# Kernel optimization log

Hardware: AMD Instinct MI355X
Metric: run time of the kernel (lower is better)

## Reference

```python
import jax, jax.numpy as jnp
import numpy as np

NINP = 1024
NHID = 1024
BATCH = 16384


def setup_inputs() -> dict:
    key = jax.random.key(0)
    ks = jax.random.split(key, 12)
    std = 1.0 / np.sqrt(NHID)
    u = lambda k, shape: jax.random.uniform(k, shape, jnp.float32, -std, std)
    return {
        "x": jax.random.normal(ks[0], (BATCH, NINP), jnp.float32),
        "y": jax.random.normal(ks[1], (BATCH, NHID), jnp.float32),
        "z": jax.random.normal(ks[2], (BATCH, NHID), jnp.float32),
        "dt": jax.random.uniform(ks[3], (BATCH, 1), jnp.float32),
        "W_ih": u(ks[4], (4 * NHID, NINP)),
        "b_ih": u(ks[5], (4 * NHID,)),
        "W_hh": u(ks[6], (3 * NHID, NHID)),
        "b_hh": u(ks[7], (3 * NHID,)),
        "W_z": u(ks[8], (NHID, NHID)),
        "b_z": u(ks[9], (NHID,)),
        "W_dt": u(ks[10], (2, 1)),
        "b_dt": u(ks[11], (2,)),
    }


def reference(x, y, z, dt, W_ih, b_ih, W_hh, b_hh, W_z, b_z, W_dt, b_dt):
    # transformed_inp = inp2hid(x): [B, 4H]
    ti = x @ W_ih.T + b_ih
    # transformed_hid = hid2hid(y): [B, 3H]
    th = y @ W_hh.T + b_hh
    H = NHID
    i_dt1, i_dt2, i_z, i_y = ti[:, :H], ti[:, H:2*H], ti[:, 2*H:3*H], ti[:, 3*H:]
    h_dt1, h_dt2, h_y = th[:, :H], th[:, H:2*H], th[:, 2*H:]
    tdt = dt @ W_dt.T + b_dt  # [B, 2]
    t_dt1, t_dt2 = tdt[:, 0:1], tdt[:, 1:2]
    ms_dt_bar = jax.nn.sigmoid(t_dt1) * jax.nn.sigmoid(i_dt1 + h_dt1)
    ms_dt = jax.nn.sigmoid(t_dt2) * jax.nn.sigmoid(i_dt2 + h_dt2)
    z_new = (1.0 - ms_dt) * z + ms_dt * jnp.tanh(i_y + h_y)
    y_new = (1.0 - ms_dt_bar) * y + ms_dt_bar * jnp.tanh(z_new @ W_z.T + b_z + i_z)
    return (y_new, z_new)
```

## Files before the change

### kernel.cpp

```cpp
#include <hip/hip_runtime.h>
#include <hip/hip_bf16.h>

#define BATCH 16384
#define HDIM  1024
#define K1    2048

typedef __attribute__((ext_vector_type(4))) float f32x4;
typedef __attribute__((ext_vector_type(4))) int i32x4;
typedef __attribute__((ext_vector_type(8))) short short8;

__device__ __forceinline__ unsigned short f2bf(float f) {
  union { float f; unsigned u; } v; v.f = f;
  unsigned r = v.u + 0x7FFFu + ((v.u >> 16) & 1u);
  return (unsigned short)(r >> 16);
}
__device__ __forceinline__ float bf2f(unsigned short h) {
  union { unsigned u; float f; } v; v.u = ((unsigned)h) << 16; return v.f;
}
__device__ __forceinline__ float sigmoidf_(float x) {
  return 1.0f / (1.0f + __builtin_amdgcn_exp2f(x * -1.4426950408889634f));
}
__device__ __forceinline__ float tanhf_(float x) {
  float xc = fminf(fmaxf(x, -8.0f), 8.0f);
  float e = __builtin_amdgcn_exp2f(xc * 2.8853900817779268f);
  return (e - 1.0f) / (e + 1.0f);
}
__device__ __forceinline__ void async16(const void* g, void* l) {
  __builtin_amdgcn_global_load_lds((const __attribute__((address_space(1))) void*)g,
                                   (__attribute__((address_space(3))) void*)l, 16, 0, 0);
}
__device__ __forceinline__ int q8p(float4 v, float s) {
  int a = __float2int_rn(fminf(fmaxf(v.x * s, -127.f), 127.f));
  int b = __float2int_rn(fminf(fmaxf(v.y * s, -127.f), 127.f));
  int c = __float2int_rn(fminf(fmaxf(v.z * s, -127.f), 127.f));
  int d = __float2int_rn(fminf(fmaxf(v.w * s, -127.f), 127.f));
  return (a & 255) | ((b & 255) << 8) | ((c & 255) << 16) | ((d & 255) << 24);
}

#define QXS (127.0f / 6.0f)
#define QWS (127.0f / 0.03125f)
#define SXW ((6.0f / 127.0f) * (0.03125f / 127.0f))

__global__ void k_conv(const float* __restrict__ x, const float* __restrict__ y,
                       const float* __restrict__ Wih, const float* __restrict__ Whh,
                       const float* __restrict__ Wz,
                       char* __restrict__ U8, unsigned short* __restrict__ Xbf,
                       char* __restrict__ W8, unsigned short* __restrict__ Wzcat) {
  const int stride = gridDim.x * blockDim.x;
  const int tid0 = blockIdx.x * blockDim.x + threadIdx.x;
  const int totalU = BATCH * (HDIM / 4);
  for (int q = tid0; q < totalU; q += stride) {
    int b = q >> 8;
    int c = (q & 255) << 2;
    float4 xv = *(const float4*)(x + (long)b * HDIM + c);
    float4 yv = *(const float4*)(y + (long)b * HDIM + c);
    *(int*)(U8 + (long)b * K1 + c) = q8p(xv, QXS);
    *(int*)(U8 + (long)b * K1 + HDIM + c) = q8p(yv, QXS);
    uint2 xo;
    xo.x = (unsigned)f2bf(xv.x) | ((unsigned)f2bf(xv.y) << 16);
    xo.y = (unsigned)f2bf(xv.z) | ((unsigned)f2bf(xv.w) << 16);
    *(uint2*)(Xbf + (long)b * HDIM + c) = xo;
  }
  const int totalW = 3072 * (K1 / 4);
  for (int q = tid0; q < totalW; q += stride) {
    int np = q >> 9;
    int kb = (q & 511) << 2;
    int bn = np / 192; int r = np - bn * 192;
    int w = r / 48; int r2 = r - w * 48;
    int c = r2 >> 4, i = r2 & 15;
    int h = bn * 64 + w * 16 + i;
    float4 v;
    if (kb < HDIM) {
      int row = (c == 0) ? h : (c == 1) ? (HDIM + h) : (3 * HDIM + h);
      v = *(const float4*)(Wih + (long)row * HDIM + kb);
    } else {
      int row = (c == 0) ? h : (c == 1) ? (HDIM + h) : (2 * HDIM + h);
      v = *(const float4*)(Whh + (long)row * HDIM + (kb - HDIM));
    }
    *(int*)(W8 + (long)np * K1 + kb) = q8p(v, QWS);
  }
  const int totalZ = HDIM * (K1 / 4);
  for (int q = tid0; q < totalZ; q += stride) {
    int n = q >> 9;
    int kb = (q & 511) << 2;
    float4 v = (kb < HDIM) ? *(const float4*)(Wz + (long)n * HDIM + kb)
                           : *(const float4*)(Wih + (long)(2 * HDIM + n) * HDIM + (kb - HDIM));
    uint2 o;
    o.x = (unsigned)f2bf(v.x) | ((unsigned)f2bf(v.y) << 16);
    o.y = (unsigned)f2bf(v.z) | ((unsigned)f2bf(v.w) << 16);
    *(uint2*)(Wzcat + (long)n * K1 + kb) = o;
  }
}

__global__ __launch_bounds__(512, 2) void k_gemm1(
    const char* __restrict__ U8, const char* __restrict__ W8,
    const float* __restrict__ z, const float* __restrict__ dtp,
    const float* __restrict__ bih, const float* __restrict__ bhh,
    const float* __restrict__ Wdt, const float* __restrict__ bdt,
    float* __restrict__ out, unsigned short* __restrict__ znb,
    unsigned short* __restrict__ sbb) {
  __shared__ char lds[114688];
  char* ldsA = lds;
  char* ldsB = lds + 65536;
  const int bid = blockIdx.x;
  const int sid = (bid & 7) * 128 + (bid >> 3);
  const int bm = sid >> 4, bn = sid & 15;
  const long arow0 = (long)bm * 256, brow0 = (long)bn * 192;
  constexpr int NT = 32;

  const int t = threadIdx.x, lane = t & 63, wv = t >> 6;
  const int wm = wv >> 2, wn = wv & 3;
  const int rA = lane & 15;
  const int cphys = ((lane >> 4) << 4) ^ (((rA >> 1) & 3) << 4);
  const int t16 = t * 16;
  const bool blo = (t < 256);

  const int sA = t16 ^ (((t16 >> 7) & 3) << 4);
  const int rA0 = sA >> 6, cA0 = sA & 63;
  const char* pAa = U8 + (arow0 + rA0) * (long)K1 + cA0;
  const char* pAb = U8 + (arow0 + rA0 + 128) * (long)K1 + cA0;

  const int Lb0 = blo ? t16 : t16 + 4096;
  const int Lb1 = t16 + 4096;
  const int sB0 = Lb0 ^ (((Lb0 >> 7) & 3) << 4);
  const int sB1 = Lb1 ^ (((Lb1 >> 7) & 3) << 4);
  const char* pBg0 = W8 + (brow0 + (sB0 >> 6)) * (long)K1 + (sB0 & 63);
  const char* pBg1 = W8 + (brow0 + (sB1 >> 6)) * (long)K1 + (sB1 & 63);

  int offA[8], offB[3];
#pragma unroll
  for (int m = 0; m < 8; ++m)
    offA[m] = (wm * 128 + m * 16 + rA) * 64 + cphys;
#pragma unroll
  for (int n = 0; n < 3; ++n)
    offB[n] = (wn * 48 + n * 16 + rA) * 64 + cphys;

#define STAGE_(TT)                                                        \
  do {                                                                    \
    char* ab_ = ldsA + ((TT) & 3) * 16384;                                \
    char* bb_ = ldsB + ((TT) & 3) * 12288;                                \
    async16(pAa + (long)(TT) * 64, ab_ + t16);                            \
    async16(pAb + (long)(TT) * 64, ab_ + 8192 + t16);                     \
    async16(pBg0 + (long)(TT) * 64, bb_ + Lb0);                           \
    if (blo) async16(pBg1 + (long)(TT) * 64, bb_ + Lb1);                  \
  } while (0)
#define WSTEADY_                                                          \
  do {                                                                    \
    if (blo) asm volatile("s_waitcnt vmcnt(8) lgkmcnt(0)" ::: "memory");  \
    else     asm volatile("s_waitcnt vmcnt(6) lgkmcnt(0)" ::: "memory");  \
  } while (0)
#define WTAIL1_                                                           \
  do {                                                                    \
    if (blo) asm volatile("s_waitcnt vmcnt(4) lgkmcnt(0)" ::: "memory");  \
    else     asm volatile("s_waitcnt vmcnt(3) lgkmcnt(0)" ::: "memory");  \
  } while (0)
#define WTAIL0_ asm volatile("s_waitcnt vmcnt(0) lgkmcnt(0)" ::: "memory")
#define WLAST_  asm volatile("s_waitcnt lgkmcnt(0)" ::: "memory")

  i32x4 acc[8][3];
#pragma unroll
  for (int m = 0; m < 8; ++m)
#pragma unroll
    for (int n = 0; n < 3; ++n) acc[m][n] = (i32x4)(0);

  STAGE_(0);
  STAGE_(1);
  STAGE_(2);
  WSTEADY_;
  __builtin_amdgcn_s_barrier();

#pragma unroll 1
  for (int kt = 0; kt < NT; ++kt) {
    const char* Ab_ = ldsA + (kt & 3) * 16384;
    const char* Bb_ = ldsB + (kt & 3) * 12288;
    i32x4 af_[8], bf_[3];
#pragma unroll
    for (int m = 0; m < 8; ++m) af_[m] = *(const i32x4*)(Ab_ + offA[m]);
#pragma unroll
    for (int n = 0; n < 3; ++n) bf_[n] = *(const i32x4*)(Bb_ + offB[n]);
    if (kt < NT - 3) {
      STAGE_(kt + 3);
      WSTEADY_;
    } else if (kt == NT - 3) {
      WTAIL1_;
    } else if (kt == NT - 2) {
      WTAIL0_;
    } else {
      WLAST_;
    }
    __builtin_amdgcn_s_barrier();
    __builtin_amdgcn_sched_barrier(0);
    __builtin_amdgcn_s_setprio(1);
#pragma unroll
    for (int m = 0; m < 8; ++m)
#pragma unroll
      for (int n = 0; n < 3; ++n)
        acc[m][n] = __builtin_amdgcn_mfma_i32_16x16x64_i8(
            af_[m], bf_[n], acc[m][n], 0, 0, 0);
    __builtin_amdgcn_s_setprio(0);
  }
#undef STAGE_
#undef WSTEADY_
#undef WTAIL1_
#undef WTAIL0_
#undef WLAST_

  const int q4 = (lane >> 4) << 2;
  const int h = bn * 64 + wn * 16 + rA;
  const int rowbase = bm * 256 + wm * 128;
  const float bi0 = bih[h] + bhh[h];
  const float bi1 = bih[HDIM + h] + bhh[HDIM + h];
  const float bi2 = bih[3 * HDIM + h] + bhh[2 * HDIM + h];
  const float wdt0 = Wdt[0], wdt1 = Wdt[1], bdt0 = bdt[0], bdt1 = bdt[1];
#pragma unroll
  for (int m = 0; m < 8; ++m) {
#pragma unroll
    for (int j = 0; j < 4; ++j) {
      const int b = rowbase + m * 16 + q4 + j;
      const long idx = (long)b * HDIM + h;
      const float dv = dtp[b];
      const float s1 = sigmoidf_(dv * wdt0 + bdt0);
      const float s2 = sigmoidf_(dv * wdt1 + bdt1);
      const float g0 = (float)acc[m][0][j] * SXW + bi0;
      const float g1 = (float)acc[m][1][j] * SXW + bi1;
      const float g2 = (float)acc[m][2][j] * SXW + bi2;
      const float sbar = s1 * sigmoidf_(g0);
      const float s = s2 * sigmoidf_(g1);
      const float zt = tanhf_(g2);
      const float znew = (1.0f - s) * z[idx] + s * zt;
      out[(long)BATCH * HDIM + idx] = znew;
      znb[idx] = f2bf(znew);
      sbb[idx] = f2bf(sbar);
    }
  }
}

template <int NB, int KSPLIT>
__device__ __forceinline__ void gemm_core(
    const unsigned short* __restrict__ A1, int strA1,
    const unsigned short* __restrict__ A2, int strA2,
    const unsigned short* __restrict__ Bg,
    long arow0, long brow0, char* lds, f32x4 acc[8][NB]) {
  constexpr int NT = 64;
  constexpr int BBY = NB * 4096;
  char* ldsA = lds;
  char* ldsB = lds + 65536;
  const int t = threadIdx.x, lane = t & 63, wv = t >> 6;
  const int wm = wv >> 2, wn = wv & 3;
  const int rA = lane & 15;
  const int cphys = ((lane >> 4) << 4) ^ (((rA >> 1) & 3) << 4);
  const int t16 = t * 16;

  const int sA = t16 ^ (((t16 >> 7) & 3) << 4);
  const int rA0 = sA >> 6, cA0 = (sA & 63) >> 1;
  const unsigned short* pA1a = A1 + (arow0 + rA0) * (long)strA1 + cA0;
  const unsigned short* pA1b = A1 + (arow0 + rA0 + 128) * (long)strA1 + cA0;
  const unsigned short* pA2a = A2 + (arow0 + rA0) * (long)strA2 + cA0;
  const unsigned short* pA2b = A2 + (arow0 + rA0 + 128) * (long)strA2 + cA0;

  const int Lb0 = t16;
  const int sB0 = Lb0 ^ (((Lb0 >> 7) & 3) << 4);
  const unsigned short* pBg0 = Bg + (brow0 + (sB0 >> 6)) * (long)K1 + ((sB0 & 63) >> 1);

  int offA[8], offB[NB];
#pragma unroll
  for (int m = 0; m < 8; ++m)
    offA[m] = (wm * 128 + m * 16 + rA) * 64 + cphys;
#pragma unroll
  for (int n = 0; n < NB; ++n)
    offB[n] = (wn * (NB * 16) + n * 16 + rA) * 64 + cphys;

#define STAGE2_(TT)                                                       \
  do {                                                                    \
    char* ab_ = ldsA + ((TT) & 3) * 16384;                                \
    char* bb_ = ldsB + ((TT) & 3) * BBY;                                  \
    if ((TT) < KSPLIT) {                                                  \
      async16(pA1a + (long)(TT) * 32, ab_ + t16);                         \
      async16(pA1b + (long)(TT) * 32, ab_ + 8192 + t16);                  \
    } else {                                                              \
      async16(pA2a + (long)((TT) - KSPLIT) * 32, ab_ + t16);              \
      async16(pA2b + (long)((TT) - KSPLIT) * 32, ab_ + 8192 + t16);       \
    }                                                                     \
    async16(pBg0 + (long)(TT) * 32, bb_ + Lb0);                           \
  } while (0)
#define W2S_ asm volatile("s_waitcnt vmcnt(6) lgkmcnt(0)" ::: "memory")
#define W2A_ asm volatile("s_waitcnt vmcnt(3) lgkmcnt(0)" ::: "memory")
#define W2B_ asm volatile("s_waitcnt vmcnt(0) lgkmcnt(0)" ::: "memory")
#define W2C_ asm volatile("s_waitcnt lgkmcnt(0)" ::: "memory")

  STAGE2_(0);
  STAGE2_(1);
  STAGE2_(2);
  W2S_;
  __builtin_amdgcn_s_barrier();

#pragma unroll 1
  for (int kt = 0; kt < NT; ++kt) {
    const char* Ab_ = ldsA + (kt & 3) * 16384;
    const char* Bb_ = ldsB + (kt & 3) * BBY;
    short8 af_[8], bf_[NB];
#pragma unroll
    for (int m = 0; m < 8; ++m) af_[m] = *(const short8*)(Ab_ + offA[m]);
#pragma unroll
    for (int n = 0; n < NB; ++n) bf_[n] = *(const short8*)(Bb_ + offB[n]);
    if (kt < NT - 3) {
      STAGE2_(kt + 3);
      W2S_;
    } else if (kt == NT - 3) {
      W2A_;
    } else if (kt == NT - 2) {
      W2B_;
    } else {
      W2C_;
    }
    __builtin_amdgcn_s_barrier();
    __builtin_amdgcn_sched_barrier(0);
    __builtin_amdgcn_s_setprio(1);
#pragma unroll
    for (int m = 0; m < 8; ++m)
#pragma unroll
      for (int n = 0; n < NB; ++n)
        acc[m][n] = __builtin_amdgcn_mfma_f32_16x16x32_bf16(
            af_[m], bf_[n], acc[m][n], 0, 0, 0);
    __builtin_amdgcn_s_setprio(0);
  }
#undef STAGE2_
#undef W2S_
#undef W2A_
#undef W2B_
#undef W2C_
}

__global__ __launch_bounds__(512, 2) void k_gemm2(
    const unsigned short* __restrict__ Zn, const unsigned short* __restrict__ Xbf,
    const unsigned short* __restrict__ Wzcat, const unsigned short* __restrict__ sbb,
    const float* __restrict__ yin, const float* __restrict__ bz,
    float* __restrict__ out) {
  __shared__ char lds[98304];
  const int bid = blockIdx.x;
  const int sid = (bid & 7) * 64 + (bid >> 3);
  const int bm = sid >> 3, bn = sid & 7;
  f32x4 acc[8][2];
#pragma unroll
  for (int m = 0; m < 8; ++m)
#pragma unroll
    for (int n = 0; n < 2; ++n) acc[m][n] = (f32x4)(0.0f);

  gemm_core<2, 32>(Zn, HDIM, Xbf, HDIM, Wzcat, (long)bm * 256, (long)bn * 128, lds, acc);

  const int t = threadIdx.x, lane = t & 63, wv = t >> 6;
  const int wm = wv >> 2, wn = wv & 3;
  const int rA = lane & 15, q4 = (lane >> 4) << 2;
  const int rowbase = bm * 256 + wm * 128;
#pragma unroll
  for (int n = 0; n < 2; ++n) {
    const int hc = bn * 128 + wn * 32 + n * 16 + rA;
    const float bzv = bz[hc];
#pragma unroll
    for (int m = 0; m < 8; ++m) {
#pragma unroll
      for (int j = 0; j < 4; ++j) {
        const int b = rowbase + m * 16 + q4 + j;
        const long idx = (long)b * HDIM + hc;
        const float tv = tanhf_(acc[m][n][j] + bzv);
        const float sb = bf2f(sbb[idx]);
        out[idx] = (1.0f - sb) * yin[idx] + sb * tv;
      }
    }
  }
}

extern "C" void kernel_launch(void* const* d_in, const int* in_sizes, int n_in,
                              void* d_out, int out_size, void* d_ws, size_t ws_size,
                              hipStream_t stream) {
  const float* x   = (const float*)d_in[0];
  const float* y   = (const float*)d_in[1];
  const float* z   = (const float*)d_in[2];
  const float* dtp = (const float*)d_in[3];
  const float* Wih = (const float*)d_in[4];
  const float* bih = (const float*)d_in[5];
  const float* Whh = (const float*)d_in[6];
  const float* bhh = (const float*)d_in[7];
  const float* Wz  = (const float*)d_in[8];
  const float* bz  = (const float*)d_in[9];
  const float* Wdt = (const float*)d_in[10];
  const float* bdt = (const float*)d_in[11];

  char* ws = (char*)d_ws;
  char*           U8    = ws;
  unsigned short* Xbf   = (unsigned short*)(ws + 33554432);
  char*           W8    = ws + 67108864;
  unsigned short* Wzcat = (unsigned short*)(ws + 73400320);
  unsigned short* Znb   = (unsigned short*)(ws + 77594624);
  unsigned short* Sbb   = (unsigned short*)(ws + 111149056);
  float* out = (float*)d_out;

  k_conv<<<2048, 256, 0, stream>>>(x, y, Wih, Whh, Wz, U8, Xbf, W8, Wzcat);
  k_gemm1<<<1024, 512, 0, stream>>>(U8, W8, z, dtp, bih, bhh, Wdt, bdt, out, Znb, Sbb);
  k_gemm2<<<512, 512, 0, stream>>>(Znb, Xbf, Wzcat, Sbb, y, bz, out);
}
```

Baseline: 324.9 us.

## Switch second GEMM to int8 MFMA and reuse quantized x from first GEMM

```diff
diff --git a/kernel.cpp b/kernel.cpp
--- a/kernel.cpp
+++ b/kernel.cpp
@@ -7,7 +7,6 @@
 
 typedef __attribute__((ext_vector_type(4))) float f32x4;
 typedef __attribute__((ext_vector_type(4))) int i32x4;
-typedef __attribute__((ext_vector_type(8))) short short8;
 
 __device__ __forceinline__ unsigned short f2bf(float f) {
   union { float f; unsigned u; } v; v.f = f;
@@ -44,8 +43,8 @@
 __global__ void k_conv(const float* __restrict__ x, const float* __restrict__ y,
                        const float* __restrict__ Wih, const float* __restrict__ Whh,
                        const float* __restrict__ Wz,
-                       char* __restrict__ U8, unsigned short* __restrict__ Xbf,
-                       char* __restrict__ W8, unsigned short* __restrict__ Wzcat) {
+                       char* __restrict__ U8, char* __restrict__ W8,
+                       char* __restrict__ Wz8) {
   const int stride = gridDim.x * blockDim.x;
   const int tid0 = blockIdx.x * blockDim.x + threadIdx.x;
   const int totalU = BATCH * (HDIM / 4);
@@ -56,10 +55,6 @@
     float4 yv = *(const float4*)(y + (long)b * HDIM + c);
     *(int*)(U8 + (long)b * K1 + c) = q8p(xv, QXS);
     *(int*)(U8 + (long)b * K1 + HDIM + c) = q8p(yv, QXS);
-    uint2 xo;
-    xo.x = (unsigned)f2bf(xv.x) | ((unsigned)f2bf(xv.y) << 16);
-    xo.y = (unsigned)f2bf(xv.z) | ((unsigned)f2bf(xv.w) << 16);
-    *(uint2*)(Xbf + (long)b * HDIM + c) = xo;
   }
   const int totalW = 3072 * (K1 / 4);
   for (int q = tid0; q < totalW; q += stride) {
@@ -85,10 +80,7 @@
     int kb = (q & 511) << 2;
     float4 v = (kb < HDIM) ? *(const float4*)(Wz + (long)n * HDIM + kb)
                            : *(const float4*)(Wih + (long)(2 * HDIM + n) * HDIM + (kb - HDIM));
-    uint2 o;
-    o.x = (unsigned)f2bf(v.x) | ((unsigned)f2bf(v.y) << 16);
-    o.y = (unsigned)f2bf(v.z) | ((unsigned)f2bf(v.w) << 16);
-    *(uint2*)(Wzcat + (long)n * K1 + kb) = o;
+    *(int*)(Wz8 + (long)n * K1 + kb) = q8p(v, QWS);
   }
 }
 
@@ -97,7 +89,7 @@
     const float* __restrict__ z, const float* __restrict__ dtp,
     const float* __restrict__ bih, const float* __restrict__ bhh,
     const float* __restrict__ Wdt, const float* __restrict__ bdt,
-    float* __restrict__ out, unsigned short* __restrict__ znb,
+    float* __restrict__ out, char* __restrict__ zn8,
     unsigned short* __restrict__ sbb) {
   __shared__ char lds[114688];
   char* ldsA = lds;
@@ -229,22 +221,27 @@
       const float zt = tanhf_(g2);
       const float znew = (1.0f - s) * z[idx] + s * zt;
       out[(long)BATCH * HDIM + idx] = znew;
-      znb[idx] = f2bf(znew);
+      int qz = __float2int_rn(fminf(fmaxf(znew * QXS, -127.f), 127.f));
+      zn8[idx] = (char)qz;
       sbb[idx] = f2bf(sbar);
     }
   }
 }
 
-template <int NB, int KSPLIT>
-__device__ __forceinline__ void gemm_core(
-    const unsigned short* __restrict__ A1, int strA1,
-    const unsigned short* __restrict__ A2, int strA2,
-    const unsigned short* __restrict__ Bg,
-    long arow0, long brow0, char* lds, f32x4 acc[8][NB]) {
-  constexpr int NT = 64;
-  constexpr int BBY = NB * 4096;
+__global__ __launch_bounds__(512, 2) void k_gemm2(
+    const char* __restrict__ Zn8, const char* __restrict__ U8,
+    const char* __restrict__ Wz8, const unsigned short* __restrict__ sbb,
+    const float* __restrict__ yin, const float* __restrict__ bz,
+    float* __restrict__ out) {
+  __shared__ char lds[98304];
   char* ldsA = lds;
   char* ldsB = lds + 65536;
+  const int bid = blockIdx.x;
+  const int sid = (bid & 7) * 64 + (bid >> 3);
+  const int bm = sid >> 3, bn = sid & 7;
+  const long arow0 = (long)bm * 256, brow0 = (long)bn * 128;
+  constexpr int NT = 32, KSPLIT = 16;
+
   const int t = threadIdx.x, lane = t & 63, wv = t >> 6;
   const int wm = wv >> 2, wn = wv & 3;
   const int rA = lane & 15;
@@ -252,42 +249,47 @@
   const int t16 = t * 16;
 
   const int sA = t16 ^ (((t16 >> 7) & 3) << 4);
-  const int rA0 = sA >> 6, cA0 = (sA & 63) >> 1;
-  const unsigned short* pA1a = A1 + (arow0 + rA0) * (long)strA1 + cA0;
-  const unsigned short* pA1b = A1 + (arow0 + rA0 + 128) * (long)strA1 + cA0;
-  const unsigned short* pA2a = A2 + (arow0 + rA0) * (long)strA2 + cA0;
-  const unsigned short* pA2b = A2 + (arow0 + rA0 + 128) * (long)strA2 + cA0;
-
-  const int Lb0 = t16;
-  const int sB0 = Lb0 ^ (((Lb0 >> 7) & 3) << 4);
-  const unsigned short* pBg0 = Bg + (brow0 + (sB0 >> 6)) * (long)K1 + ((sB0 & 63) >> 1);
-
-  int offA[8], offB[NB];
+  const int rA0 = sA >> 6, cA0 = sA & 63;
+  const char* pZa = Zn8 + (arow0 + rA0) * (long)HDIM + cA0;
+  const char* pZb = Zn8 + (arow0 + rA0 + 128) * (long)HDIM + cA0;
+  const char* pXa = U8 + (arow0 + rA0) * (long)K1 + cA0;
+  const char* pXb = U8 + (arow0 + rA0 + 128) * (long)K1 + cA0;
+
+  const int sB0 = t16 ^ (((t16 >> 7) & 3) << 4);
+  const char* pBg0 = Wz8 + (brow0 + (sB0 >> 6)) * (long)K1 + (sB0 & 63);
+
+  int offA[8], offB[2];
 #pragma unroll
   for (int m = 0; m < 8; ++m)
     offA[m] = (wm * 128 + m * 16 + rA) * 64 + cphys;
 #pragma unroll
-  for (int n = 0; n < NB; ++n)
-    offB[n] = (wn * (NB * 16) + n * 16 + rA) * 64 + cphys;
+  for (int n = 0; n < 2; ++n)
+    offB[n] = (wn * 32 + n * 16 + rA) * 64 + cphys;
 
 #define STAGE2_(TT)                                                       \
   do {                                                                    \
     char* ab_ = ldsA + ((TT) & 3) * 16384;                                \
-    char* bb_ = ldsB + ((TT) & 3) * BBY;                                  \
+    char* bb_ = ldsB + ((TT) & 3) * 8192;                                 \
     if ((TT) < KSPLIT) {                                                  \
-      async16(pA1a + (long)(TT) * 32, ab_ + t16);                         \
-      async16(pA1b + (long)(TT) * 32, ab_ + 8192 + t16);                  \
+      async16(pZa + (long)(TT) * 64, ab_ + t16);                          \
+      async16(pZb + (long)(TT) * 64, ab_ + 8192 + t16);                   \
     } else {                                                              \
-      async16(pA2a + (long)((TT) - KSPLIT) * 32, ab_ + t16);              \
-      async16(pA2b + (long)((TT) - KSPLIT) * 32, ab_ + 8192 + t16);       \
+      async16(pXa + (long)((TT) - KSPLIT) * 64, ab_ + t16);               \
+      async16(pXb + (long)((TT) - KSPLIT) * 64, ab_ + 8192 + t16);        \
     }                                                                     \
-    async16(pBg0 + (long)(TT) * 32, bb_ + Lb0);                           \
+    async16(pBg0 + (long)(TT) * 64, bb_ + t16);                           \
   } while (0)
 #define W2S_ asm volatile("s_waitcnt vmcnt(6) lgkmcnt(0)" ::: "memory")
 #define W2A_ asm volatile("s_waitcnt vmcnt(3) lgkmcnt(0)" ::: "memory")
 #define W2B_ asm volatile("s_waitcnt vmcnt(0) lgkmcnt(0)" ::: "memory")
 #define W2C_ asm volatile("s_waitcnt lgkmcnt(0)" ::: "memory")
 
+  i32x4 acc[8][2];
+#pragma unroll
+  for (int m = 0; m < 8; ++m)
+#pragma unroll
+    for (int n = 0; n < 2; ++n) acc[m][n] = (i32x4)(0);
+
   STAGE2_(0);
   STAGE2_(1);
   STAGE2_(2);
@@ -297,12 +299,12 @@
 #pragma unroll 1
   for (int kt = 0; kt < NT; ++kt) {
     const char* Ab_ = ldsA + (kt & 3) * 16384;
-    const char* Bb_ = ldsB + (kt & 3) * BBY;
-    short8 af_[8], bf_[NB];
-#pragma unroll
-    for (int m = 0; m < 8; ++m) af_[m] = *(const short8*)(Ab_ + offA[m]);
-#pragma unroll
-    for (int n = 0; n < NB; ++n) bf_[n] = *(const short8*)(Bb_ + offB[n]);
+    const char* Bb_ = ldsB + (kt & 3) * 8192;
+    i32x4 af_[8], bf_[2];
+#pragma unroll
+    for (int m = 0; m < 8; ++m) af_[m] = *(const i32x4*)(Ab_ + offA[m]);
+#pragma unroll
+    for (int n = 0; n < 2; ++n) bf_[n] = *(const i32x4*)(Bb_ + offB[n]);
     if (kt < NT - 3) {
       STAGE2_(kt + 3);
       W2S_;
@@ -319,8 +321,8 @@
 #pragma unroll
     for (int m = 0; m < 8; ++m)
 #pragma unroll
-      for (int n = 0; n < NB; ++n)
-        acc[m][n] = __builtin_amdgcn_mfma_f32_16x16x32_bf16(
+      for (int n = 0; n < 2; ++n)
+        acc[m][n] = __builtin_amdgcn_mfma_i32_16x16x64_i8(
             af_[m], bf_[n], acc[m][n], 0, 0, 0);
     __builtin_amdgcn_s_setprio(0);
   }
@@ -329,28 +331,8 @@
 #undef W2A_
 #undef W2B_
 #undef W2C_
-}
-
-__global__ __launch_bounds__(512, 2) void k_gemm2(
-    const unsigned short* __restrict__ Zn, const unsigned short* __restrict__ Xbf,
-    const unsigned short* __restrict__ Wzcat, const unsigned short* __restrict__ sbb,
-    const float* __restrict__ yin, const float* __restrict__ bz,
-    float* __restrict__ out) {
-  __shared__ char lds[98304];
-  const int bid = blockIdx.x;
-  const int sid = (bid & 7) * 64 + (bid >> 3);
-  const int bm = sid >> 3, bn = sid & 7;
-  f32x4 acc[8][2];
-#pragma unroll
-  for (int m = 0; m < 8; ++m)
-#pragma unroll
-    for (int n = 0; n < 2; ++n) acc[m][n] = (f32x4)(0.0f);
-
-  gemm_core<2, 32>(Zn, HDIM, Xbf, HDIM, Wzcat, (long)bm * 256, (long)bn * 128, lds, acc);
-
-  const int t = threadIdx.x, lane = t & 63, wv = t >> 6;
-  const int wm = wv >> 2, wn = wv & 3;
-  const int rA = lane & 15, q4 = (lane >> 4) << 2;
+
+  const int q4 = (lane >> 4) << 2;
   const int rowbase = bm * 256 + wm * 128;
 #pragma unroll
   for (int n = 0; n < 2; ++n) {
@@ -362,7 +344,7 @@
       for (int j = 0; j < 4; ++j) {
         const int b = rowbase + m * 16 + q4 + j;
         const long idx = (long)b * HDIM + hc;
-        const float tv = tanhf_(acc[m][n][j] + bzv);
+        const float tv = tanhf_((float)acc[m][n][j] * SXW + bzv);
         const float sb = bf2f(sbb[idx]);
         out[idx] = (1.0f - sb) * yin[idx] + sb * tv;
       }
@@ -387,15 +369,14 @@
   const float* bdt = (const float*)d_in[11];
 
   char* ws = (char*)d_ws;
-  char*           U8    = ws;
-  unsigned short* Xbf   = (unsigned short*)(ws + 33554432);
-  char*           W8    = ws + 67108864;
-  unsigned short* Wzcat = (unsigned short*)(ws + 73400320);
-  unsigned short* Znb   = (unsigned short*)(ws + 77594624);
-  unsigned short* Sbb   = (unsigned short*)(ws + 111149056);
+  char*           U8  = ws;
+  char*           W8  = ws + 33554432;
+  char*           Wz8 = ws + 39845888;
+  char*           Zn8 = ws + 41943040;
+  unsigned short* Sbb = (unsigned short*)(ws + 58720256);
   float* out = (float*)d_out;
 
-  k_conv<<<2048, 256, 0, stream>>>(x, y, Wih, Whh, Wz, U8, Xbf, W8, Wzcat);
-  k_gemm1<<<1024, 512, 0, stream>>>(U8, W8, z, dtp, bih, bhh, Wdt, bdt, out, Znb, Sbb);
-  k_gemm2<<<512, 512, 0, stream>>>(Znb, Xbf, Wzcat, Sbb, y, bz, out);
-}
+  k_conv<<<2048, 256, 0, stream>>>(x, y, Wih, Whh, Wz, U8, W8, Wz8);
+  k_gemm1<<<1024, 512, 0, stream>>>(U8, W8, z, dtp, bih, bhh, Wdt, bdt, out, Zn8, Sbb);
+  k_gemm2<<<512, 512, 0, stream>>>(Zn8, U8, Wz8, Sbb, y, bz, out);
+}
```

New measurement: 262.0 us. 19.4% less time.
